# Kernel tuning notes

Hardware: AMD Instinct MI355X
Metric: run time of the kernel (lower is better)

The kernel has to match this reference:

```python
import jax, jax.numpy as jnp
import numpy as np

B, S, E, H = 4, 2048, 1024, 16
D = E // H  # head_dim = 64

def setup_inputs() -> dict:
    key = jax.random.key(0)
    k1, k2, k3 = jax.random.split(key, 3)
    x = jax.random.normal(k1, (B, S, E), dtype=jnp.float32)
    # Linear weights stored as [in, out] so y = x @ W (torch Linear uses W^T; same math).
    w_att = jax.random.normal(k2, (E, 3 * E), dtype=jnp.float32) * (1.0 / np.sqrt(E))
    w_proj = jax.random.normal(k3, (E, E), dtype=jnp.float32) * (1.0 / np.sqrt(E))
    return {"x": x, "w_att": w_att, "w_proj": w_proj}

def reference(x, w_att, w_proj):
    b, s, e = x.shape
    qkv = x @ w_att                      # [b, s, 3e]
    q, k, v = jnp.split(qkv, 3, axis=-1)
    # [b, h, s, d]
    q = q.reshape(b, s, H, D).transpose(0, 2, 1, 3)
    k = k.reshape(b, s, H, D).transpose(0, 2, 1, 3)
    v = v.reshape(b, s, H, D).transpose(0, 2, 1, 3)
    scale = 1.0 / np.sqrt(D)
    att = jnp.einsum('bhqd,bhkd->bhqk', q, k) * scale  # [b, h, s, s]
    causal = jnp.tril(jnp.ones((s, s), dtype=bool))
    att = jnp.where(causal[None, None], att, jnp.finfo(att.dtype).min)
    att = jax.nn.softmax(att, axis=-1)
    y = jnp.einsum('bhqk,bhkd->bhqd', att, v)          # [b, h, s, d]
    y = y.transpose(0, 2, 1, 3).reshape(b, s, e)
    return y @ w_proj
```

## Files before the change

### kernel.cpp

```cpp
#include <hip/hip_runtime.h>
#include <hip/hip_bf16.h>

typedef __bf16 b16v8 __attribute__((ext_vector_type(8)));
typedef __bf16 b16v4 __attribute__((ext_vector_type(4)));
typedef float  f32x4 __attribute__((ext_vector_type(4)));

#define BB 4
#define SS 2048
#define EE 1024
#define HH 16
#define DD 64

#define QSCALE 0.18033688011112042f
#define CMAX 20.0f

__device__ __forceinline__ void async16(const __bf16* g, __bf16* l) {
  typedef __attribute__((address_space(1))) const unsigned int gu32;
  typedef __attribute__((address_space(3))) unsigned int lu32;
  __builtin_amdgcn_global_load_lds((gu32*)g, (lu32*)l, 16, 0, 0);
}

__device__ __forceinline__ f32x4 mfma16x16x16_bf16(b16v4 a, b16v4 b, f32x4 c) {
#if __has_builtin(__builtin_amdgcn_mfma_f32_16x16x16_bf16)
  return __builtin_amdgcn_mfma_f32_16x16x16_bf16(a, b, c, 0, 0, 0);
#else
  typedef short s16v4 __attribute__((ext_vector_type(4)));
  union U { b16v4 h; s16v4 s; };
  U ua, ub; ua.h = a; ub.h = b;
  return __builtin_amdgcn_mfma_f32_16x16x16bf16_1k(ua.s, ub.s, c, 0, 0, 0);
#endif
}

__global__ __launch_bounds__(256) void cast_x_kernel(const float* __restrict__ in,
                                                     __bf16* __restrict__ out, int n4) {
  int i = blockIdx.x * 256 + threadIdx.x;
  if (i >= n4) return;
  float4 f = ((const float4*)in)[i];
  b16v4 o = {(__bf16)f.x, (__bf16)f.y, (__bf16)f.z, (__bf16)f.w};
  ((b16v4*)out)[i] = o;
}

__global__ __launch_bounds__(256) void cast_transpose(const float* __restrict__ w,
                                                      __bf16* __restrict__ wt, int K, int N) {
  __shared__ float t[32][33];
  int n0 = blockIdx.x * 32, k0 = blockIdx.y * 32;
  int tx = threadIdx.x & 31, ty = threadIdx.x >> 5;
#pragma unroll
  for (int j = 0; j < 32; j += 8)
    t[ty + j][tx] = w[(size_t)(k0 + ty + j) * N + n0 + tx];
  __syncthreads();
#pragma unroll
  for (int j = 0; j < 32; j += 8)
    wt[(size_t)(n0 + ty + j) * K + k0 + tx] = (__bf16)t[tx][ty + j];
}

template <int EPI>
__global__ __launch_bounds__(512, 2) void gemm256(const __bf16* __restrict__ A,
                                                  const __bf16* __restrict__ Bt,
                                                  void* C0, void* C1, void* C2,
                                                  int M, int N, int K) {
  __shared__ __bf16 lds[2][32768];
  const int tid = threadIdx.x;
  const int lane = tid & 63;
  const int wid = tid >> 6;
  const int wm = (wid >> 2) * 128;
  const int wn = (wid & 3) * 64;
  const int l16 = lane & 15, quad = lane >> 4;

  const int gx = gridDim.x, gy = gridDim.y;
  const int nwg = gx * gy;
  const int bid = blockIdx.y * gx + blockIdx.x;
  const int qq = nwg >> 3, rr = nwg & 7;
  const int xcd = bid & 7, idx = bid >> 3;
  const int wgid = (xcd < rr ? xcd * (qq + 1) : rr * (qq + 1) + (xcd - rr) * qq) + idx;
  const int bx = wgid % gx, by = wgid / gx;

  const __bf16* Ab = A + (size_t)by * 256 * K;
  const __bf16* Bb = Bt + (size_t)bx * 256 * K;

  const __bf16 *sA[4], *sB[4];
  int ldst[4];
#pragma unroll
  for (int h = 0; h < 2; ++h)
#pragma unroll
    for (int i = 0; i < 2; ++i) {
      int L = tid + i * 512;
      int row = L >> 3, c = L & 7;
      int sw = (c ^ (row & 7)) * 8;
      sA[h * 2 + i] = Ab + (size_t)(h * 128 + row) * K + sw;
      sB[h * 2 + i] = Bb + (size_t)(h * 128 + row) * K + sw;
      ldst[h * 2 + i] = h * 8192 + L * 8;
    }
  auto stageA = [&](int bi, int t) {
#pragma unroll
    for (int j = 0; j < 4; ++j) async16(sA[j] + (t << 6), &lds[bi][ldst[j]]);
  };
  auto stageB = [&](int bi, int t) {
#pragma unroll
    for (int j = 0; j < 4; ++j) async16(sB[j] + (t << 6), &lds[bi][16384 + ldst[j]]);
  };

  const int aB = (wm + l16) * 64;
  const int bB = 16384 + (wn + l16) * 64;
  const int e7 = l16 & 7;
  const int swz0 = (quad ^ e7) * 8;
  const int swz1 = ((4 + quad) ^ e7) * 8;

  f32x4 acc[8][4];
#pragma unroll
  for (int i = 0; i < 8; ++i)
#pragma unroll
    for (int j = 0; j < 4; ++j) acc[i][j] = f32x4{0.f, 0.f, 0.f, 0.f};

  stageA(0, 0);
  stageB(0, 0);
  asm volatile("s_waitcnt vmcnt(0)" ::: "memory");
  __builtin_amdgcn_s_barrier();

  const int KT = K >> 6;
  for (int kt = 0; kt < KT; ++kt) {
    const __bf16* bufp = lds[kt & 1];
    const int nb = (kt + 1) & 1;
    const bool more = (kt + 1) < KT;
    b16v8 a[4][2], b0[2][2], b1[2][2];

#pragma unroll
    for (int mt = 0; mt < 4; ++mt) {
      a[mt][0] = *(const b16v8*)(bufp + aB + mt * 1024 + swz0);
      a[mt][1] = *(const b16v8*)(bufp + aB + mt * 1024 + swz1);
    }
#pragma unroll
    for (int nt = 0; nt < 2; ++nt) {
      b0[nt][0] = *(const b16v8*)(bufp + bB + nt * 1024 + swz0);
      b0[nt][1] = *(const b16v8*)(bufp + bB + nt * 1024 + swz1);
    }
    if (more) stageA(nb, kt + 1);
    __builtin_amdgcn_s_barrier();
    asm volatile("s_waitcnt lgkmcnt(0)" ::: "memory");
    __builtin_amdgcn_s_setprio(1);
#pragma unroll
    for (int mt = 0; mt < 4; ++mt)
#pragma unroll
      for (int nt = 0; nt < 2; ++nt)
#pragma unroll
        for (int ks = 0; ks < 2; ++ks)
          acc[mt][nt] = __builtin_amdgcn_mfma_f32_16x16x32_bf16(a[mt][ks], b0[nt][ks], acc[mt][nt], 0, 0, 0);
    __builtin_amdgcn_s_setprio(0);
    __builtin_amdgcn_s_barrier();

#pragma unroll
    for (int nt = 0; nt < 2; ++nt) {
      b1[nt][0] = *(const b16v8*)(bufp + bB + (2 + nt) * 1024 + swz0);
      b1[nt][1] = *(const b16v8*)(bufp + bB + (2 + nt) * 1024 + swz1);
    }
    if (more) stageB(nb, kt + 1);
    __builtin_amdgcn_s_barrier();
    asm volatile("s_waitcnt lgkmcnt(0)" ::: "memory");
    __builtin_amdgcn_s_setprio(1);
#pragma unroll
    for (int mt = 0; mt < 4; ++mt)
#pragma unroll
      for (int nt = 0; nt < 2; ++nt)
#pragma unroll
        for (int ks = 0; ks < 2; ++ks)
          acc[mt][2 + nt] = __builtin_amdgcn_mfma_f32_16x16x32_bf16(a[mt][ks], b1[nt][ks], acc[mt][2 + nt], 0, 0, 0);
    __builtin_amdgcn_s_setprio(0);
    __builtin_amdgcn_s_barrier();

#pragma unroll
    for (int mt = 0; mt < 4; ++mt) {
      a[mt][0] = *(const b16v8*)(bufp + aB + 4096 + mt * 1024 + swz0);
      a[mt][1] = *(const b16v8*)(bufp + aB + 4096 + mt * 1024 + swz1);
    }
    __builtin_amdgcn_s_barrier();
    asm volatile("s_waitcnt lgkmcnt(0)" ::: "memory");
    __builtin_amdgcn_s_setprio(1);
#pragma unroll
    for (int mt = 0; mt < 4; ++mt)
#pragma unroll
      for (int nt = 0; nt < 2; ++nt)
#pragma unroll
        for (int ks = 0; ks < 2; ++ks)
          acc[4 + mt][2 + nt] = __builtin_amdgcn_mfma_f32_16x16x32_bf16(a[mt][ks], b1[nt][ks], acc[4 + mt][2 + nt], 0, 0, 0);
    __builtin_amdgcn_s_setprio(0);
    __builtin_amdgcn_s_barrier();

    __builtin_amdgcn_s_setprio(1);
#pragma unroll
    for (int mt = 0; mt < 4; ++mt)
#pragma unroll
      for (int nt = 0; nt < 2; ++nt)
#pragma unroll
        for (int ks = 0; ks < 2; ++ks)
          acc[4 + mt][nt] = __builtin_amdgcn_mfma_f32_16x16x32_bf16(a[mt][ks], b0[nt][ks], acc[4 + mt][nt], 0, 0, 0);
    __builtin_amdgcn_s_setprio(0);
    asm volatile("s_waitcnt vmcnt(0)" ::: "memory");
    __builtin_amdgcn_s_barrier();
  }

  if (EPI == 0) {
    __bf16* qb = (__bf16*)C0;
    __bf16* kb = (__bf16*)C1;
    __bf16* vtb = (__bf16*)C2;
#pragma unroll
    for (int mt = 0; mt < 8; ++mt)
#pragma unroll
      for (int nt = 0; nt < 4; ++nt) {
        int row = by * 256 + wm + mt * 16 + quad * 4;
        int col = bx * 256 + wn + nt * 16 + l16;
        int b = row >> 11, s = row & 2047;
        int sec = col >> 10, cc = col & 1023;
        int h = cc >> 6, d = cc & 63;
        if (sec == 2) {
          b16v4 vv = {(__bf16)acc[mt][nt][0], (__bf16)acc[mt][nt][1],
                      (__bf16)acc[mt][nt][2], (__bf16)acc[mt][nt][3]};
          *(b16v4*)(vtb + ((size_t)(b * HH + h) * DD + d) * SS + s) = vv;
        } else {
          __bf16* dst = (sec == 0) ? qb : kb;
          float sc = (sec == 0) ? QSCALE : 1.0f;
#pragma unroll
          for (int r = 0; r < 4; ++r)
            dst[(((size_t)(b * HH + h) * SS + s + r) << 6) + d] = (__bf16)(acc[mt][nt][r] * sc);
        }
      }
  } else {
    float* out = (float*)C0;
#pragma unroll
    for (int mt = 0; mt < 8; ++mt)
#pragma unroll
      for (int nt = 0; nt < 4; ++nt) {
        int row = by * 256 + wm + mt * 16 + quad * 4;
        int col = bx * 256 + wn + nt * 16 + l16;
#pragma unroll
        for (int r = 0; r < 4; ++r)
          out[(size_t)(row + r) * N + col] = acc[mt][nt][r];
      }
  }
}

__global__ __launch_bounds__(256, 4) void attn_kernel(const __bf16* __restrict__ qb,
                                                      const __bf16* __restrict__ kb,
                                                      const __bf16* __restrict__ vtb,
                                                      __bf16* __restrict__ y) {
  __shared__ __bf16 kv_lds[2][8192];
  const int tid = threadIdx.x;
  const int lane = tid & 63;
  const int w = tid >> 6;
  const int l16 = lane & 15, quad = lane >> 4;
  const int bh = blockIdx.x, p = blockIdx.y;
  const int b = bh >> 4, h = bh & 15;
  const __bf16* kbase = kb + (size_t)bh * SS * DD;
  const __bf16* vtbase = vtb + (size_t)bh * DD * SS;

  const int e = l16 & 7;
  const int koff0 = l16 * 64 + ((quad ^ e) * 8);
  const int koff1 = l16 * 64 + (((quad + 4) ^ e) * 8);
  int voff[4];
#pragma unroll
  for (int kf = 0; kf < 4; ++kf)
    voff[kf] = 4096 + l16 * 64 + (((kf * 2 + (quad >> 1)) ^ e) * 8) + ((quad & 1) * 4);

  int gK[2], gV[2], lK[2], lV[2];
#pragma unroll
  for (int i = 0; i < 2; ++i) {
    int L = tid + i * 256;
    int row = L >> 3, c = L & 7;
    gK[i] = row * DD + ((c ^ (row & 7)) * 8);
    lK[i] = L * 8;
    gV[i] = row * SS + ((c ^ (row & 7)) * 8);
    lV[i] = 4096 + L * 8;
  }
  auto stage = [&](int j, __bf16* buf) {
    const __bf16* kj = kbase + j * (64 * DD);
    const __bf16* vj = vtbase + j * 64;
#pragma unroll
    for (int i = 0; i < 2; ++i) async16(kj + gK[i], buf + lK[i]);
#pragma unroll
    for (int i = 0; i < 2; ++i) async16(vj + gV[i], buf + lV[i]);
  };

#pragma unroll
  for (int t = 0; t < 2; ++t) {
    const int qt = (t == 0) ? (31 - p) : p;

    b16v8 qf[2];
#pragma unroll
    for (int ks = 0; ks < 2; ++ks)
      qf[ks] = *(const b16v8*)(qb + ((size_t)bh * SS + qt * 64 + w * 16 + l16) * DD + ks * 32 + quad * 8);

    f32x4 o[4];
#pragma unroll
    for (int dt = 0; dt < 4; ++dt) o[dt] = f32x4{0.f, 0.f, 0.f, 0.f};
    f32x4 lv = {0.f, 0.f, 0.f, 0.f};

    __syncthreads();
    stage(0, kv_lds[0]);

    for (int j = 0; j <= qt; ++j) {
      __syncthreads();
      if (j < qt) stage(j + 1, kv_lds[(j + 1) & 1]);
      const __bf16* buf = kv_lds[0] + ((j & 1) << 13);

      f32x4 s[4];
#pragma unroll
      for (int kf = 0; kf < 4; ++kf) s[kf] = f32x4{-CMAX, -CMAX, -CMAX, -CMAX};
#pragma unroll
      for (int kf = 0; kf < 4; ++kf) {
        b16v8 k0 = *(const b16v8*)(buf + koff0 + kf * 1024);
        b16v8 k1 = *(const b16v8*)(buf + koff1 + kf * 1024);
        s[kf] = __builtin_amdgcn_mfma_f32_16x16x32_bf16(k0, qf[0], s[kf], 0, 0, 0);
        s[kf] = __builtin_amdgcn_mfma_f32_16x16x32_bf16(k1, qf[1], s[kf], 0, 0, 0);
      }
      if (j == qt) {
        int ql = w * 16 + l16;
#pragma unroll
        for (int kf = 0; kf < 4; ++kf)
#pragma unroll
          for (int r = 0; r < 4; ++r)
            if (kf * 16 + quad * 4 + r > ql) s[kf][r] = -1e30f;
      }
#pragma unroll
      for (int kf = 0; kf < 4; ++kf)
#pragma unroll
        for (int r = 0; r < 4; ++r) s[kf][r] = __builtin_amdgcn_exp2f(s[kf][r]);
      lv += (s[0] + s[1]) + (s[2] + s[3]);
#pragma unroll
      for (int kf = 0; kf < 4; ++kf) {
        b16v4 pf = {(__bf16)s[kf][0], (__bf16)s[kf][1], (__bf16)s[kf][2], (__bf16)s[kf][3]};
#pragma unroll
        for (int dt = 0; dt < 4; ++dt) {
          b16v4 vf = *(const b16v4*)(buf + voff[kf] + dt * 1024);
          o[dt] = mfma16x16x16_bf16(vf, pf, o[dt]);
        }
      }
    }

    float lr = (lv[0] + lv[1]) + (lv[2] + lv[3]);
    lr += __shfl_xor(lr, 16);
    lr += __shfl_xor(lr, 32);
    float inv = 1.0f / lr;
    int q = qt * 64 + w * 16 + l16;
#pragma unroll
    for (int dt = 0; dt < 4; ++dt) {
      b16v4 ov = {(__bf16)(o[dt][0] * inv), (__bf16)(o[dt][1] * inv),
                  (__bf16)(o[dt][2] * inv), (__bf16)(o[dt][3] * inv)};
      *(b16v4*)(y + ((size_t)b * SS + q) * EE + h * 64 + dt * 16 + quad * 4) = ov;
    }
  }
}

extern "C" void kernel_launch(void* const* d_in, const int* in_sizes, int n_in,
                              void* d_out, int out_size, void* d_ws, size_t ws_size,
                              hipStream_t stream) {
  (void)in_sizes; (void)n_in; (void)out_size; (void)ws_size;
  const float* x = (const float*)d_in[0];
  const float* w_att = (const float*)d_in[1];
  const float* w_proj = (const float*)d_in[2];
  float* out = (float*)d_out;

  char* ws = (char*)d_ws;
  size_t off = 0;
  auto alloc = [&](size_t elems) { __bf16* p = (__bf16*)(ws + off); off += elems * 2; return p; };
  __bf16* xb = alloc(8388608);
  __bf16* qb = alloc(8388608);
  __bf16* kb = alloc(8388608);
  __bf16* vtb = alloc(8388608);
  __bf16* watt = alloc(3145728);
  __bf16* wproj = alloc(1048576);

  cast_x_kernel<<<8192, 256, 0, stream>>>(x, xb, 2097152);
  cast_transpose<<<dim3(96, 32), 256, 0, stream>>>(w_att, watt, 1024, 3072);
  cast_transpose<<<dim3(32, 32), 256, 0, stream>>>(w_proj, wproj, 1024, 1024);
  gemm256<0><<<dim3(12, 32), 512, 0, stream>>>(xb, watt, qb, kb, vtb, 8192, 3072, 1024);
  attn_kernel<<<dim3(64, 16), 256, 0, stream>>>(qb, kb, vtb, xb);
  gemm256<1><<<dim3(4, 32), 512, 0, stream>>>(xb, wproj, out, nullptr, nullptr, 8192, 1024, 1024);
}
```

Baseline: 250.7 us.

## Split GEMM tile loads into half-stages and overlap with MFMA phases

The GEMM's A and B LDS staging is split into two halves each, with the shared-memory layout reordered so that each compute phase needs only one half. Each half is issued at a separate point in the four-phase MFMA schedule and waited on with partial vmcnt counts, replacing the single full drain at the end of each k-tile. The last k-tile is specialised at compile time so it issues no prefetch. This is meant to hide global-to-LDS latency behind MFMA work, at the cost of more fragile hand-written waitcnt accounting and a remapped epilogue indexing.

```diff
diff --git a/kernel.cpp b/kernel.cpp
--- a/kernel.cpp
+++ b/kernel.cpp
@@ -4,6 +4,8 @@
 typedef __bf16 b16v8 __attribute__((ext_vector_type(8)));
 typedef __bf16 b16v4 __attribute__((ext_vector_type(4)));
 typedef float  f32x4 __attribute__((ext_vector_type(4)));
+
+template <bool B> struct BoolC { static constexpr bool value = B; };
 
 #define BB 4
 #define SS 2048
@@ -63,12 +65,11 @@
   const int tid = threadIdx.x;
   const int lane = tid & 63;
   const int wid = tid >> 6;
-  const int wm = (wid >> 2) * 128;
-  const int wn = (wid & 3) * 64;
+  const int wm01 = wid >> 2, wn01 = wid & 3;
   const int l16 = lane & 15, quad = lane >> 4;
 
-  const int gx = gridDim.x, gy = gridDim.y;
-  const int nwg = gx * gy;
+  const int gx = gridDim.x;
+  const int nwg = gx * gridDim.y;
   const int bid = blockIdx.y * gx + blockIdx.x;
   const int qq = nwg >> 3, rr = nwg & 7;
   const int xcd = bid & 7, idx = bid >> 3;
@@ -78,30 +79,33 @@
   const __bf16* Ab = A + (size_t)by * 256 * K;
   const __bf16* Bb = Bt + (size_t)bx * 256 * K;
 
-  const __bf16 *sA[4], *sB[4];
-  int ldst[4];
-#pragma unroll
-  for (int h = 0; h < 2; ++h)
-#pragma unroll
-    for (int i = 0; i < 2; ++i) {
-      int L = tid + i * 512;
-      int row = L >> 3, c = L & 7;
-      int sw = (c ^ (row & 7)) * 8;
-      sA[h * 2 + i] = Ab + (size_t)(h * 128 + row) * K + sw;
-      sB[h * 2 + i] = Bb + (size_t)(h * 128 + row) * K + sw;
-      ldst[h * 2 + i] = h * 8192 + L * 8;
-    }
-  auto stageA = [&](int bi, int t) {
-#pragma unroll
-    for (int j = 0; j < 4; ++j) async16(sA[j] + (t << 6), &lds[bi][ldst[j]]);
+  const __bf16 *sA[2][2], *sB[2][2];
+  int ldst[2];
+#pragma unroll
+  for (int i = 0; i < 2; ++i) {
+    int L = tid + i * 512;
+    int r = L >> 3, c = L & 7;
+    int sw = (c ^ (r & 7)) * 8;
+    ldst[i] = L * 8;
+#pragma unroll
+    for (int h = 0; h < 2; ++h) {
+      int ra = (r >> 6) * 128 + h * 64 + (r & 63);
+      int rb = (r >> 5) * 64 + h * 32 + (r & 31);
+      sA[h][i] = Ab + (size_t)ra * K + sw;
+      sB[h][i] = Bb + (size_t)rb * K + sw;
+    }
+  }
+  auto stageA = [&](int bi, int t, int h) {
+#pragma unroll
+    for (int i = 0; i < 2; ++i) async16(sA[h][i] + (t << 6), &lds[bi][h * 8192 + ldst[i]]);
   };
-  auto stageB = [&](int bi, int t) {
-#pragma unroll
-    for (int j = 0; j < 4; ++j) async16(sB[j] + (t << 6), &lds[bi][16384 + ldst[j]]);
+  auto stageB = [&](int bi, int t, int h) {
+#pragma unroll
+    for (int i = 0; i < 2; ++i) async16(sB[h][i] + (t << 6), &lds[bi][16384 + h * 8192 + ldst[i]]);
   };
 
-  const int aB = (wm + l16) * 64;
-  const int bB = 16384 + (wn + l16) * 64;
+  const int aB = (wm01 * 64 + l16) * 64;
+  const int bB = 16384 + (wn01 * 32 + l16) * 64;
   const int e7 = l16 & 7;
   const int swz0 = (quad ^ e7) * 8;
   const int swz1 = ((4 + quad) ^ e7) * 8;
@@ -112,29 +116,32 @@
 #pragma unroll
     for (int j = 0; j < 4; ++j) acc[i][j] = f32x4{0.f, 0.f, 0.f, 0.f};
 
-  stageA(0, 0);
-  stageB(0, 0);
-  asm volatile("s_waitcnt vmcnt(0)" ::: "memory");
+  stageA(0, 0, 0);
+  stageB(0, 0, 0);
+  stageB(0, 0, 1);
+  stageA(0, 0, 1);
+  asm volatile("s_waitcnt vmcnt(4)" ::: "memory");
   __builtin_amdgcn_s_barrier();
 
   const int KT = K >> 6;
-  for (int kt = 0; kt < KT; ++kt) {
-    const __bf16* bufp = lds[kt & 1];
-    const int nb = (kt + 1) & 1;
-    const bool more = (kt + 1) < KT;
+  auto ktile = [&](int t, auto moreC) {
+    constexpr bool MORE = decltype(moreC)::value;
+    const __bf16* cur = lds[t & 1];
+    const int nb = (t + 1) & 1;
     b16v8 a[4][2], b0[2][2], b1[2][2];
 
 #pragma unroll
     for (int mt = 0; mt < 4; ++mt) {
-      a[mt][0] = *(const b16v8*)(bufp + aB + mt * 1024 + swz0);
-      a[mt][1] = *(const b16v8*)(bufp + aB + mt * 1024 + swz1);
+      a[mt][0] = *(const b16v8*)(cur + aB + mt * 1024 + swz0);
+      a[mt][1] = *(const b16v8*)(cur + aB + mt * 1024 + swz1);
     }
 #pragma unroll
     for (int nt = 0; nt < 2; ++nt) {
-      b0[nt][0] = *(const b16v8*)(bufp + bB + nt * 1024 + swz0);
-      b0[nt][1] = *(const b16v8*)(bufp + bB + nt * 1024 + swz1);
-    }
-    if (more) stageA(nb, kt + 1);
+      b0[nt][0] = *(const b16v8*)(cur + bB + nt * 1024 + swz0);
+      b0[nt][1] = *(const b16v8*)(cur + bB + nt * 1024 + swz1);
+    }
+    if constexpr (MORE) stageA(nb, t + 1, 0);
+    asm volatile("s_waitcnt lgkmcnt(8)" ::: "memory");
     __builtin_amdgcn_s_barrier();
     asm volatile("s_waitcnt lgkmcnt(0)" ::: "memory");
     __builtin_amdgcn_s_setprio(1);
@@ -146,14 +153,16 @@
         for (int ks = 0; ks < 2; ++ks)
           acc[mt][nt] = __builtin_amdgcn_mfma_f32_16x16x32_bf16(a[mt][ks], b0[nt][ks], acc[mt][nt], 0, 0, 0);
     __builtin_amdgcn_s_setprio(0);
+    if constexpr (MORE) asm volatile("s_waitcnt vmcnt(4)" ::: "memory");
+    else                asm volatile("s_waitcnt vmcnt(2)" ::: "memory");
     __builtin_amdgcn_s_barrier();
 
 #pragma unroll
     for (int nt = 0; nt < 2; ++nt) {
-      b1[nt][0] = *(const b16v8*)(bufp + bB + (2 + nt) * 1024 + swz0);
-      b1[nt][1] = *(const b16v8*)(bufp + bB + (2 + nt) * 1024 + swz1);
-    }
-    if (more) stageB(nb, kt + 1);
+      b1[nt][0] = *(const b16v8*)(cur + bB + 8192 + nt * 1024 + swz0);
+      b1[nt][1] = *(const b16v8*)(cur + bB + 8192 + nt * 1024 + swz1);
+    }
+    if constexpr (MORE) stageB(nb, t + 1, 0);
     __builtin_amdgcn_s_barrier();
     asm volatile("s_waitcnt lgkmcnt(0)" ::: "memory");
     __builtin_amdgcn_s_setprio(1);
@@ -165,13 +174,16 @@
         for (int ks = 0; ks < 2; ++ks)
           acc[mt][2 + nt] = __builtin_amdgcn_mfma_f32_16x16x32_bf16(a[mt][ks], b1[nt][ks], acc[mt][2 + nt], 0, 0, 0);
     __builtin_amdgcn_s_setprio(0);
+    if constexpr (MORE) asm volatile("s_waitcnt vmcnt(4)" ::: "memory");
+    else                asm volatile("s_waitcnt vmcnt(0)" ::: "memory");
     __builtin_amdgcn_s_barrier();
 
 #pragma unroll
     for (int mt = 0; mt < 4; ++mt) {
-      a[mt][0] = *(const b16v8*)(bufp + aB + 4096 + mt * 1024 + swz0);
-      a[mt][1] = *(const b16v8*)(bufp + aB + 4096 + mt * 1024 + swz1);
-    }
+      a[mt][0] = *(const b16v8*)(cur + aB + 8192 + mt * 1024 + swz0);
+      a[mt][1] = *(const b16v8*)(cur + aB + 8192 + mt * 1024 + swz1);
+    }
+    if constexpr (MORE) stageB(nb, t + 1, 1);
     __builtin_amdgcn_s_barrier();
     asm volatile("s_waitcnt lgkmcnt(0)" ::: "memory");
     __builtin_amdgcn_s_setprio(1);
@@ -185,6 +197,7 @@
     __builtin_amdgcn_s_setprio(0);
     __builtin_amdgcn_s_barrier();
 
+    if constexpr (MORE) stageA(nb, t + 1, 1);
     __builtin_amdgcn_s_setprio(1);
 #pragma unroll
     for (int mt = 0; mt < 4; ++mt)
@@ -194,9 +207,12 @@
         for (int ks = 0; ks < 2; ++ks)
           acc[4 + mt][nt] = __builtin_amdgcn_mfma_f32_16x16x32_bf16(a[mt][ks], b0[nt][ks], acc[4 + mt][nt], 0, 0, 0);
     __builtin_amdgcn_s_setprio(0);
-    asm volatile("s_waitcnt vmcnt(0)" ::: "memory");
-    __builtin_amdgcn_s_barrier();
-  }
+    if constexpr (MORE) asm volatile("s_waitcnt vmcnt(4)" ::: "memory");
+    __builtin_amdgcn_s_barrier();
+  };
+
+  for (int t = 0; t < KT - 1; ++t) ktile(t, BoolC<true>{});
+  ktile(KT - 1, BoolC<false>{});
 
   if (EPI == 0) {
     __bf16* qb = (__bf16*)C0;
@@ -206,8 +222,8 @@
     for (int mt = 0; mt < 8; ++mt)
 #pragma unroll
       for (int nt = 0; nt < 4; ++nt) {
-        int row = by * 256 + wm + mt * 16 + quad * 4;
-        int col = bx * 256 + wn + nt * 16 + l16;
+        int row = by * 256 + wm01 * 128 + (mt >> 2) * 64 + (mt & 3) * 16 + quad * 4;
+        int col = bx * 256 + wn01 * 64 + (nt >> 1) * 32 + (nt & 1) * 16 + l16;
         int b = row >> 11, s = row & 2047;
         int sec = col >> 10, cc = col & 1023;
         int h = cc >> 6, d = cc & 63;
@@ -229,8 +245,8 @@
     for (int mt = 0; mt < 8; ++mt)
 #pragma unroll
       for (int nt = 0; nt < 4; ++nt) {
-        int row = by * 256 + wm + mt * 16 + quad * 4;
-        int col = bx * 256 + wn + nt * 16 + l16;
+        int row = by * 256 + wm01 * 128 + (mt >> 2) * 64 + (mt & 3) * 16 + quad * 4;
+        int col = bx * 256 + wn01 * 64 + (nt >> 1) * 32 + (nt & 1) * 16 + l16;
 #pragma unroll
         for (int r = 0; r < 4; ++r)
           out[(size_t)(row + r) * N + col] = acc[mt][nt][r];
```

Measured after the change: 245.0 us. 2.3% less time.
